# Performance work log

Measured on AMD Instinct MI355X. Metric: run time of the kernel, lower is better.

## Reference

```python
import jax, jax.numpy as jnp
import numpy as np

B, T, C = 2, 2048, 1024
H = 16
D = C // H  # head_dim = 64
EPS = 1e-06
MAX_SEQ = 2048


def make_rotary(dim, max_seq_len, base=10000):
    inv_freq = 1.0 / (base ** (jnp.arange(0, dim, 2, dtype=jnp.float32) / dim))
    pos = jnp.arange(max_seq_len, dtype=jnp.float32)
    sinusoid = jnp.einsum('i,j->ij', pos, inv_freq)  # (S, dim//2)
    return jnp.sin(sinusoid), jnp.cos(sinusoid)


def apply_rotary(x, sin, cos):
    # x: (B, T, H, D); sin/cos: (MAX_SEQ, D//2)
    t = x.shape[1]
    s = sin[:t][:, None, :]  # (T,1,D//2) broadcasts over B and H
    c = cos[:t][:, None, :]
    d = x.shape[-1]
    x1, x2 = x[..., :d // 2], x[..., d // 2:]
    return jnp.concatenate([x1 * c - x2 * s, x2 * c + x1 * s], axis=-1)


def yat_dense(x, kernel, bias, alpha, eps=EPS):
    # Yat layer: squared dot product over squared euclidean distance.
    dot = x @ kernel                                   # (..., out)
    x_sq = jnp.sum(x * x, axis=-1, keepdims=True)      # (..., 1)
    k_sq = jnp.sum(kernel * kernel, axis=0)            # (out,)
    dist = x_sq + k_sq - 2.0 * dot
    y = (dot * dot) / (dist + eps)
    out_f = kernel.shape[1]
    scale = (jnp.sqrt(jnp.float32(out_f)) / jnp.log(1.0 + jnp.float32(out_f))) ** alpha
    return y * scale + bias


def setup_inputs() -> dict:
    key = jax.random.key(0)
    ks = jax.random.split(key, 7)
    x = jax.random.normal(ks[0], (B, T, C), dtype=jnp.float32)
    mask = jnp.tril(jnp.ones((T, T), dtype=bool))[None].repeat(B, axis=0)  # (B,T,T) causal
    s = 1.0 / np.sqrt(C)
    w_attn = jax.random.normal(ks[1], (C, 3 * C), dtype=jnp.float32) * s
    b_attn = jnp.zeros((3 * C,), dtype=jnp.float32)
    a_attn = jnp.ones((1,), dtype=jnp.float32)
    w_proj = jax.random.normal(ks[2], (C, C), dtype=jnp.float32) * s
    b_proj = jnp.zeros((C,), dtype=jnp.float32)
    a_proj = jnp.ones((1,), dtype=jnp.float32)
    return {"x": x, "mask": mask, "w_attn": w_attn, "b_attn": b_attn,
            "a_attn": a_attn, "w_proj": w_proj, "b_proj": b_proj, "a_proj": a_proj}


def reference(x, mask, w_attn, b_attn, a_attn, w_proj, b_proj, a_proj):
    b, t, c = x.shape
    sin, cos = make_rotary(D, MAX_SEQ)
    qkv = yat_dense(x, w_attn, b_attn, a_attn)          # (B,T,3C)
    qkv = qkv.reshape(b, t, 3, H, D)
    q, k, v = jnp.moveaxis(qkv, 2, 0)                   # each (B,T,H,D)
    q = apply_rotary(q, sin, cos)
    k = apply_rotary(k, sin, cos)
    # heads-major layout for attention
    q = q.transpose(0, 2, 1, 3)                          # (B,H,T,D)
    k = k.transpose(0, 2, 1, 3)
    v = v.transpose(0, 2, 1, 3)
    scale = jnp.sqrt(jnp.float32(D))
    attn = jnp.einsum('bhqd,bhkd->bhqk', q, k) / scale   # (B,H,T,T)
    m = mask[:, None, :, :]                              # (B,1,T,T)
    attn = jnp.where(m, attn, jnp.finfo(jnp.float32).min)
    attn = jax.nn.softmax(attn, axis=-1)
    # dropout is identity in deterministic/eval mode
    out = jnp.einsum('bhqk,bhkd->bhqd', attn, v)         # (B,H,T,D)
    out = out.transpose(0, 2, 1, 3).reshape(b, t, c)     # (B,T,C)
    out = yat_dense(out, w_proj, b_proj, a_proj)
    return out
```

## Files before the change

kernel.cpp:

```cpp
#include <hip/hip_runtime.h>
#include <math.h>

#define TSEQ  2048
#define BATCH 2
#define NH    16
#define HD    64
#define CDIM  1024
#define N3C   3072
#define EPSY  1e-6f

typedef unsigned short u16;
typedef unsigned int u32;
typedef __attribute__((ext_vector_type(2))) unsigned int u32x2;
typedef __attribute__((ext_vector_type(8))) short bf16x8;
typedef __attribute__((ext_vector_type(4))) float f32x4;

#define MFMA16(a, b, c) __builtin_amdgcn_mfma_f32_16x16x32_bf16(a, b, c, 0, 0, 0)

__device__ __forceinline__ u16 f2bf(float f) {
    unsigned u = __float_as_uint(f);
    return (u16)((u + 0x7fffu + ((u >> 16) & 1u)) >> 16);
}
__device__ __forceinline__ u32 cvtpk_bf16(float lo, float hi) {
    u32 r;
    asm("v_cvt_pk_bf16_f32 %0, %1, %2" : "=v"(r) : "v"(lo), "v"(hi));
    return r;
}
__device__ __forceinline__ void gload16(const void* g, void* l) {
    __builtin_amdgcn_global_load_lds(
        (const __attribute__((address_space(1))) unsigned int*)g,
        (__attribute__((address_space(3))) unsigned int*)l, 16, 0, 0);
}

__global__ __launch_bounds__(256) void prep_kernel(
    const float* __restrict__ x, const float* __restrict__ wa,
    const float* __restrict__ wp, u16* __restrict__ Ahi,
    u16* __restrict__ Wthi, u16* __restrict__ Wphi,
    float* __restrict__ ksq, float* __restrict__ xsq,
    float* __restrict__ osq, float2* __restrict__ ropeSC) {
    __shared__ float smem[64 * 68];
    int bid = blockIdx.x, tid = threadIdx.x;

    if (bid < 4096) {
        int lane = tid & 63, wv = tid >> 6;
        size_t base = (size_t)bid * CDIM + tid * 4;
        float4 v = *(const float4*)(x + base);
        ushort4 hi;
        hi.x = f2bf(v.x); hi.y = f2bf(v.y); hi.z = f2bf(v.z); hi.w = f2bf(v.w);
        *(ushort4*)(Ahi + base) = hi;
        float s = v.x * v.x + v.y * v.y + v.z * v.z + v.w * v.w;
        #pragma unroll
        for (int off = 32; off; off >>= 1) s += __shfl_down(s, off, 64);
        if (lane == 0) smem[wv] = s;
        __syncthreads();
        if (tid == 0) xsq[bid] = smem[0] + smem[1] + smem[2] + smem[3];
    } else if (bid < 5120) {
        const float* W; u16* Whi; int K, N, bx, by;
        if (bid < 4864) {
            int t = bid - 4096; W = wa; Whi = Wthi; K = CDIM; N = N3C;
            bx = t % 48; by = t / 48;
        } else {
            int t = bid - 4864; W = wp; Whi = Wphi; K = CDIM; N = CDIM;
            bx = t % 16; by = t / 16;
        }
        int k0 = by * 64, n0 = bx * 64;
        int r = tid >> 4, c4 = (tid & 15) * 4;
        #pragma unroll
        for (int i = 0; i < 4; ++i) {
            int k = k0 + r + i * 16;
            float4 v = *(const float4*)(W + (size_t)k * N + n0 + c4);
            *(float4*)&smem[(r + i * 16) * 68 + c4] = v;
        }
        __syncthreads();
        int n = tid >> 4, k4 = (tid & 15) * 4;
        #pragma unroll
        for (int i = 0; i < 4; ++i) {
            int nn = n + i * 16;
            ushort4 hi;
            hi.x = f2bf(smem[(k4 + 0) * 68 + nn]);
            hi.y = f2bf(smem[(k4 + 1) * 68 + nn]);
            hi.z = f2bf(smem[(k4 + 2) * 68 + nn]);
            hi.w = f2bf(smem[(k4 + 3) * 68 + nn]);
            *(ushort4*)(Whi + (size_t)(n0 + nn) * K + k0 + k4) = hi;
        }
    } else if (bid < 5184) {
        int b2 = bid - 5120;
        int c = tid & 63, kq = tid >> 6;
        const float* W; int N, col, outoff;
        if (b2 < 48) { W = wa; N = N3C;  col = b2 * 64 + c;        outoff = 0;   }
        else         { W = wp; N = CDIM; col = (b2 - 48) * 64 + c; outoff = N3C; }
        float s = 0.f;
        int i0 = kq * 256;
        #pragma unroll 4
        for (int i = i0; i < i0 + 256; ++i) {
            float v = W[(size_t)i * N + col];
            s = fmaf(v, v, s);
        }
        smem[tid] = s;
        __syncthreads();
        if (kq == 0)
            ksq[outoff + col] = smem[c] + smem[64 + c] + smem[128 + c] + smem[192 + c];
    } else {
        int idx = (bid - 5184) * 256 + tid;
        if (idx < BATCH * TSEQ) osq[idx] = 0.f;
        int t = idx >> 5, j = idx & 31;
        float inv = exp2f(-(float)j * 0.4152410118609203f);
        float ang = (float)t * inv;
        ropeSC[idx] = make_float2(cosf(ang), sinf(ang));
    }
}

__global__ __launch_bounds__(256, 4) void gemm1_fused(
    const u16* __restrict__ Ah, const u16* __restrict__ Bh,
    const float* __restrict__ bias, const float* __restrict__ rowsq,
    const float* __restrict__ colsq, const float* __restrict__ alphap,
    const float2* __restrict__ ropeSC,
    u16* __restrict__ Qb, u16* __restrict__ Kb, u16* __restrict__ Vt) {
    constexpr int BK = 32;
    const int K = CDIM;
    __shared__ u16 Ash[2][128 * BK], Bsh[2][128 * BK];
    int tid = threadIdx.x;
    int lane = tid & 63, wv = tid >> 6;
    int quad = lane >> 4, l15 = lane & 15;
    int wr = wv >> 1, wc = wv & 1;
    int bm = blockIdx.y * 128, bn = blockIdx.x * 128;
    int rsub = lane >> 2;
    int lc8 = (lane & 3) * 8;
    int gc8 = (((lane & 3) - (rsub >> 1)) & 3) * 8;
    int pf8 = ((quad + (l15 >> 1)) & 3) * 8;

    f32x4 acc[4][4];
    #pragma unroll
    for (int i = 0; i < 4; ++i)
        #pragma unroll
        for (int j = 0; j < 4; ++j) acc[i][j] = (f32x4){0.f, 0.f, 0.f, 0.f};

    auto STAGE = [&](int buf, int kt) {
        #pragma unroll
        for (int i = 0; i < 2; ++i) {
            int r = i * 64 + wv * 16 + rsub;
            gload16(Ah + (size_t)(bm + r) * K + kt + gc8, &Ash[buf][r * BK + lc8]);
            gload16(Bh + (size_t)(bn + r) * K + kt + gc8, &Bsh[buf][r * BK + lc8]);
        }
    };

    STAGE(0, 0);
    __syncthreads();
    int cur = 0;

    for (int kt = 0; kt < K; kt += BK) {
        if (kt + BK < K) STAGE(cur ^ 1, kt + BK);
        bf16x8 fah[4], fbh[4];
        #pragma unroll
        for (int i = 0; i < 4; ++i)
            fah[i] = *(const bf16x8*)&Ash[cur][(wr * 64 + i * 16 + l15) * BK + pf8];
        #pragma unroll
        for (int j = 0; j < 4; ++j)
            fbh[j] = *(const bf16x8*)&Bsh[cur][(wc * 64 + j * 16 + l15) * BK + pf8];
        #pragma unroll
        for (int i = 0; i < 4; ++i)
            #pragma unroll
            for (int j = 0; j < 4; ++j)
                acc[i][j] = MFMA16(fah[i], fbh[j], acc[i][j]);
        __syncthreads();
        cur ^= 1;
    }

    float alpha = alphap[0];
    float scale = powf(sqrtf((float)N3C) / logf(1.0f + (float)N3C), alpha);
    int segc0 = bn + wc * 64;
    int seg = segc0 >> 10;
    int h = (segc0 >> 6) & 15;
    int bglob = bm >> 11;
    int bh = bglob * NH + h;

    if (seg < 2) {
        u16* dst = (seg == 0) ? Qb : Kb;
        float qs = (seg == 0) ? 0.18033688011112043f : 1.0f;
        #pragma unroll
        for (int i = 0; i < 4; ++i) {
            int tb = bm + wr * 64 + i * 16 + quad * 4;
            #pragma unroll
            for (int r = 0; r < 4; ++r) {
                int row = tb + r;
                int t = row & (TSEQ - 1);
                float rs = rowsq[row];
                float y[4];
                #pragma unroll
                for (int j = 0; j < 4; ++j) {
                    int col = segc0 + j * 16 + l15;
                    float dot = acc[i][j][r];
                    float dist = rs + colsq[col] - 2.0f * dot + EPSY;
                    y[j] = dot * dot / dist * scale + bias[col];
                }
                float2 sc0 = ropeSC[t * 32 + l15];
                float2 sc1 = ropeSC[t * 32 + 16 + l15];
                float c0 = sc0.x, s0 = sc0.y, c1 = sc1.x, s1 = sc1.y;
                size_t ob = ((size_t)bh * TSEQ + t) * HD;
                dst[ob + l15]      = f2bf((y[0] * c0 - y[2] * s0) * qs);
                dst[ob + 16 + l15] = f2bf((y[1] * c1 - y[3] * s1) * qs);
                dst[ob + 32 + l15] = f2bf((y[2] * c0 + y[0] * s0) * qs);
                dst[ob + 48 + l15] = f2bf((y[3] * c1 + y[1] * s1) * qs);
            }
        }
    } else {
        #pragma unroll
        for (int i = 0; i < 4; ++i) {
            int tb = bm + wr * 64 + i * 16 + quad * 4;
            int t0 = tb & (TSEQ - 1);
            #pragma unroll
            for (int j = 0; j < 4; ++j) {
                int col = segc0 + j * 16 + l15;
                int d = j * 16 + l15;
                float cs = colsq[col], bi = bias[col];
                ushort4 pk;
                u16* pp = (u16*)&pk;
                #pragma unroll
                for (int r = 0; r < 4; ++r) {
                    float dot = acc[i][j][r];
                    float dist = rowsq[tb + r] + cs - 2.0f * dot + EPSY;
                    pp[r] = f2bf(dot * dot / dist * scale + bi);
                }
                *(ushort4*)(Vt + ((size_t)bh * HD + d) * TSEQ + t0) = pk;
            }
        }
    }
}

__global__ __launch_bounds__(256, 4) void gemm_yat_mfma(
    const u16* __restrict__ Ah, const u16* __restrict__ Bh,
    const float* __restrict__ bias, const float* __restrict__ rowsq,
    const float* __restrict__ colsq, const float* __restrict__ alphap,
    float* __restrict__ outp, int M, int N, int K, float outf) {
    constexpr int BM = 128, BN = 64, BK = 32;
    __shared__ u16 Ash[2][BM * BK], Bsh[2][BN * BK];
    int tid = threadIdx.x;
    int lane = tid & 63, wv = tid >> 6;
    int quad = lane >> 4, l15 = lane & 15;
    int bm = blockIdx.y * BM, bn = blockIdx.x * BN;
    int rsub = lane >> 2;
    int lc8 = (lane & 3) * 8;
    int gc8 = (((lane & 3) - (rsub >> 1)) & 3) * 8;
    int pf8 = ((quad + (l15 >> 1)) & 3) * 8;

    f32x4 acc[2][4];
    #pragma unroll
    for (int i = 0; i < 2; ++i)
        #pragma unroll
        for (int j = 0; j < 4; ++j) acc[i][j] = (f32x4){0.f, 0.f, 0.f, 0.f};

    auto STAGE = [&](int buf, int kt) {
        #pragma unroll
        for (int i = 0; i < 2; ++i) {
            int r = i * 64 + wv * 16 + rsub;
            gload16(Ah + (size_t)(bm + r) * K + kt + gc8, &Ash[buf][r * BK + lc8]);
        }
        {
            int r = wv * 16 + rsub;
            gload16(Bh + (size_t)(bn + r) * K + kt + gc8, &Bsh[buf][r * BK + lc8]);
        }
    };

    STAGE(0, 0);
    __syncthreads();
    int cur = 0;

    for (int kt = 0; kt < K; kt += BK) {
        if (kt + BK < K) STAGE(cur ^ 1, kt + BK);
        bf16x8 fah[2], fbh[4];
        #pragma unroll
        for (int i = 0; i < 2; ++i)
            fah[i] = *(const bf16x8*)&Ash[cur][(wv * 32 + i * 16 + l15) * BK + pf8];
        #pragma unroll
        for (int j = 0; j < 4; ++j)
            fbh[j] = *(const bf16x8*)&Bsh[cur][(j * 16 + l15) * BK + pf8];
        #pragma unroll
        for (int i = 0; i < 2; ++i)
            #pragma unroll
            for (int j = 0; j < 4; ++j)
                acc[i][j] = MFMA16(fah[i], fbh[j], acc[i][j]);
        __syncthreads();
        cur ^= 1;
    }

    float alpha = alphap[0];
    float scale = powf(sqrtf(outf) / logf(1.0f + outf), alpha);
    #pragma unroll
    for (int j = 0; j < 4; ++j) {
        int col = bn + j * 16 + l15;
        float cs = colsq[col], bi = bias[col];
        #pragma unroll
        for (int i = 0; i < 2; ++i) {
            #pragma unroll
            for (int r = 0; r < 4; ++r) {
                int row = bm + wv * 32 + i * 16 + quad * 4 + r;
                float dot = acc[i][j][r];
                float dist = rowsq[row] + cs - 2.0f * dot + EPSY;
                outp[(size_t)row * N + col] = dot * dot / dist * scale + bi;
            }
        }
    }
}

__global__ __launch_bounds__(512) void attn_mfma(
    const u16* __restrict__ Qb, const u16* __restrict__ Kb,
    const u16* __restrict__ Vt, u16* __restrict__ Chi,
    float* __restrict__ osq) {
    __shared__ u16 Ksh[2][64 * 64];
    __shared__ u16 Vsh[2][64 * 64];
    int tid = threadIdx.x;
    int lane = tid & 63, wv = tid >> 6;
    int quad = lane >> 4, l15 = lane & 15;
    const bool oddq = (quad & 1) != 0;
    int bh = blockIdx.x;
    int b = bh >> 4, h = bh & 15;
    const u16* Qh = Qb + (size_t)bh * TSEQ * HD;
    const u16* Kh = Kb + (size_t)bh * TSEQ * HD;
    const u16* Vh = Vt + (size_t)bh * HD * TSEQ;
    const f32x4 zf = {0.f, 0.f, 0.f, 0.f};

    int qbb = 15 - blockIdx.y;
    int qw = qbb * 128 + wv * 16;
    int NT = 2 * qbb + 2;
    bf16x8 bq0 = *(const bf16x8*)(Qh + (size_t)(qw + l15) * HD + quad * 8);
    bf16x8 bq1 = *(const bf16x8*)(Qh + (size_t)(qw + l15) * HD + 32 + quad * 8);

    f32x4 o[4] = {zf, zf, zf, zf};
    float l = 0.f;

    auto STAGE = [&](int buf, int kt) {
        int k0s = kt * 64;
        int rowi = tid >> 3, ch = tid & 7;
        int gk = (ch + rowi) & 7;
        gload16(Kh + (size_t)(k0s + rowi) * HD + gk * 8, &Ksh[buf][tid * 8]);
        gload16(Vh + (size_t)rowi * TSEQ + k0s + gk * 8, &Vsh[buf][tid * 8]);
    };

    STAGE(0, 0);
    __syncthreads();
    int cur = 0;

    for (int kt = 0; kt < NT; ++kt) {
        int k0 = kt * 64;
        if (kt + 1 < NT) STAGE(cur ^ 1, kt + 1);
        if (k0 <= qw + 15) {
            const u16* Kc = Ksh[cur];
            const u16* Vc = Vsh[cur];

            f32x4 st[4];
            __builtin_amdgcn_s_setprio(1);
            #pragma unroll
            for (int mt = 0; mt < 4; ++mt) {
                int key = mt * 16 + l15;
                bf16x8 a0 = *(const bf16x8*)&Kc[key * 64 + ((quad - key) & 7) * 8];
                bf16x8 a1 = *(const bf16x8*)&Kc[key * 64 + ((4 + quad - key) & 7) * 8];
                st[mt] = MFMA16(a0, bq0, zf);
                st[mt] = MFMA16(a1, bq1, st[mt]);
            }
            __builtin_amdgcn_s_setprio(0);
            if (k0 + 63 > qw) {
                int q = qw + l15;
                #pragma unroll
                for (int mt = 0; mt < 4; ++mt)
                    #pragma unroll
                    for (int r = 0; r < 4; ++r)
                        if (k0 + mt * 16 + quad * 4 + r > q) st[mt][r] = -1e30f;
            }
            u32 pp[4][2];
            #pragma unroll
            for (int mt = 0; mt < 4; ++mt) {
                float p0 = __builtin_amdgcn_exp2f(st[mt][0]);
                float p1 = __builtin_amdgcn_exp2f(st[mt][1]);
                float p2 = __builtin_amdgcn_exp2f(st[mt][2]);
                float p3 = __builtin_amdgcn_exp2f(st[mt][3]);
                l += (p0 + p1) + (p2 + p3);
                pp[mt][0] = cvtpk_bf16(p0, p1);
                pp[mt][1] = cvtpk_bf16(p2, p3);
            }
            #pragma unroll
            for (int s = 0; s < 2; ++s) {
                u32x2 r0 = __builtin_amdgcn_permlane32_swap(
                    pp[2 * s][0], pp[2 * s + 1][0], false, false);
                u32 sA0 = (u32)__builtin_amdgcn_ds_swizzle((int)r0.x, 0x401F);
                u32 sB0 = (u32)__builtin_amdgcn_ds_swizzle((int)r0.y, 0x401F);
                u32x2 r1 = __builtin_amdgcn_permlane32_swap(
                    pp[2 * s][1], pp[2 * s + 1][1], false, false);
                u32 sA1 = (u32)__builtin_amdgcn_ds_swizzle((int)r1.x, 0x401F);
                u32 sB1 = (u32)__builtin_amdgcn_ds_swizzle((int)r1.y, 0x401F);
                u32 bw0 = oddq ? sB0 : r0.x;
                u32 bw1 = oddq ? sB1 : r1.x;
                u32 bw2 = oddq ? r0.y : sA0;
                u32 bw3 = oddq ? r1.y : sA1;
                bf16x8 bfr;
                *(u32*)&((short*)&bfr)[0] = bw0;
                *(u32*)&((short*)&bfr)[2] = bw1;
                *(u32*)&((short*)&bfr)[4] = bw2;
                *(u32*)&((short*)&bfr)[6] = bw3;
                __builtin_amdgcn_s_setprio(1);
                #pragma unroll
                for (int dt = 0; dt < 4; ++dt) {
                    int d = dt * 16 + l15;
                    bf16x8 av = *(const bf16x8*)&Vc[d * 64 + ((s * 4 + quad - d) & 7) * 8];
                    o[dt] = MFMA16(av, bfr, o[dt]);
                }
                __builtin_amdgcn_s_setprio(0);
            }
        }
        __syncthreads();
        cur ^= 1;
    }

    l += __shfl_xor(l, 16, 64);
    l += __shfl_xor(l, 32, 64);
    float inv = 1.0f / l;
    int row = (b << 11) + qw + l15;
    float ss = 0.f;
    #pragma unroll
    for (int dt = 0; dt < 4; ++dt) {
        float v0 = o[dt][0] * inv, v1 = o[dt][1] * inv;
        float v2 = o[dt][2] * inv, v3 = o[dt][3] * inv;
        ss += v0 * v0 + v1 * v1 + v2 * v2 + v3 * v3;
        uint2 pk2;
        pk2.x = cvtpk_bf16(v0, v1);
        pk2.y = cvtpk_bf16(v2, v3);
        *(uint2*)(Chi + (size_t)row * CDIM + h * HD + dt * 16 + quad * 4) = pk2;
    }
    ss += __shfl_xor(ss, 16, 64);
    ss += __shfl_xor(ss, 32, 64);
    if (quad == 0) atomicAdd(osq + row, ss);
}

extern "C" void kernel_launch(void* const* d_in, const int* in_sizes, int n_in,
                              void* d_out, int out_size, void* d_ws, size_t ws_size,
                              hipStream_t stream) {
    const float* x      = (const float*)d_in[0];
    const float* w_attn = (const float*)d_in[2];
    const float* b_attn = (const float*)d_in[3];
    const float* a_attn = (const float*)d_in[4];
    const float* w_proj = (const float*)d_in[5];
    const float* b_proj = (const float*)d_in[6];
    const float* a_proj = (const float*)d_in[7];
    float* outp = (float*)d_out;

    char* ws = (char*)d_ws;
    float* ksq = (float*)(ws);
    float* xsq = (float*)(ws + 16384);
    float* osq = (float*)(ws + 32768);
    char* pA  = ws + 65536;
    u16* Ahi = (u16*)pA;
    u16* Chi = (u16*)pA;
    char* pWt = pA + 16777216;
    u16* Wthi = (u16*)pWt;
    char* pWp = pWt + 6291456;
    u16* Wphi = (u16*)pWp;
    char* pQ = pWp + 2097152;
    u16* Qb = (u16*)pQ;
    u16* Kb = (u16*)(pQ + 8388608);
    u16* Vt = (u16*)(pQ + 16777216);
    float2* ropeSC = (float2*)(pQ + 25165824);

    prep_kernel<<<5440, 256, 0, stream>>>(
        x, w_attn, w_proj, Ahi, Wthi, Wphi, ksq, xsq, osq, ropeSC);
    gemm1_fused<<<dim3(N3C / 128, (BATCH * TSEQ) / 128), 256, 0, stream>>>(
        Ahi, Wthi, b_attn, xsq, ksq, a_attn, ropeSC, Qb, Kb, Vt);
    attn_mfma<<<dim3(BATCH * NH, 16), 512, 0, stream>>>(Qb, Kb, Vt, Chi, osq);
    gemm_yat_mfma<<<dim3(CDIM / 64, (BATCH * TSEQ) / 128), 256, 0, stream>>>(
        Chi, Wphi, b_proj, osq, ksq + N3C, a_proj, outp,
        BATCH * TSEQ, CDIM, CDIM, (float)CDIM);
}
```

Before: 225.6 us.

## Retile QKV GEMM to 128x64 blocks with two waves and swizzle block order

The fused QKV GEMM now uses 128x64 output tiles computed by 128-thread blocks (two waves, each owning 64 rows). This doubles the grid to 1536 blocks so more of the machine's CUs get work. Both GEMMs also remap the linear block index with a stride-8 swizzle, which changes which blocks run together and is meant to improve L2 reuse of the A and B tiles. In exchange each block carries a smaller B tile, so operand reuse per block drops and total global traffic rises.

```diff
diff --git a/kernel.cpp b/kernel.cpp
--- a/kernel.cpp
+++ b/kernel.cpp
@@ -110,7 +110,7 @@
     }
 }
 
-__global__ __launch_bounds__(256, 4) void gemm1_fused(
+__global__ __launch_bounds__(128, 3) void gemm1_fused(
     const u16* __restrict__ Ah, const u16* __restrict__ Bh,
     const float* __restrict__ bias, const float* __restrict__ rowsq,
     const float* __restrict__ colsq, const float* __restrict__ alphap,
@@ -118,15 +118,20 @@
     u16* __restrict__ Qb, u16* __restrict__ Kb, u16* __restrict__ Vt) {
     constexpr int BK = 32;
     const int K = CDIM;
-    __shared__ u16 Ash[2][128 * BK], Bsh[2][128 * BK];
+    __shared__ u16 Ash[2][128 * BK], Bsh[2][64 * BK];
     int tid = threadIdx.x;
     int lane = tid & 63, wv = tid >> 6;
     int quad = lane >> 4, l15 = lane & 15;
-    int wr = wv >> 1, wc = wv & 1;
-    int bm = blockIdx.y * 128, bn = blockIdx.x * 128;
-    int rsub = lane >> 2;
-    int lc8 = (lane & 3) * 8;
-    int gc8 = (((lane & 3) - (rsub >> 1)) & 3) * 8;
+
+    int lin = blockIdx.x + blockIdx.y * 48;
+    int swz = (lin & 7) * 192 + (lin >> 3);
+    int bn = (swz % 48) * 64;
+    int bm = (swz / 48) * 128;
+
+    int rs = tid >> 2;
+    int cc = tid & 3;
+    int lc8 = cc * 8;
+    int gc8 = ((cc - ((rs & 15) >> 1)) & 3) * 8;
     int pf8 = ((quad + (l15 >> 1)) & 3) * 8;
 
     f32x4 acc[4][4];
@@ -137,9 +142,13 @@
 
     auto STAGE = [&](int buf, int kt) {
         #pragma unroll
-        for (int i = 0; i < 2; ++i) {
-            int r = i * 64 + wv * 16 + rsub;
+        for (int p = 0; p < 4; ++p) {
+            int r = p * 32 + rs;
             gload16(Ah + (size_t)(bm + r) * K + kt + gc8, &Ash[buf][r * BK + lc8]);
+        }
+        #pragma unroll
+        for (int p = 0; p < 2; ++p) {
+            int r = p * 32 + rs;
             gload16(Bh + (size_t)(bn + r) * K + kt + gc8, &Bsh[buf][r * BK + lc8]);
         }
     };
@@ -153,10 +162,10 @@
         bf16x8 fah[4], fbh[4];
         #pragma unroll
         for (int i = 0; i < 4; ++i)
-            fah[i] = *(const bf16x8*)&Ash[cur][(wr * 64 + i * 16 + l15) * BK + pf8];
+            fah[i] = *(const bf16x8*)&Ash[cur][(wv * 64 + i * 16 + l15) * BK + pf8];
         #pragma unroll
         for (int j = 0; j < 4; ++j)
-            fbh[j] = *(const bf16x8*)&Bsh[cur][(wc * 64 + j * 16 + l15) * BK + pf8];
+            fbh[j] = *(const bf16x8*)&Bsh[cur][(j * 16 + l15) * BK + pf8];
         #pragma unroll
         for (int i = 0; i < 4; ++i)
             #pragma unroll
@@ -168,7 +177,7 @@
 
     float alpha = alphap[0];
     float scale = powf(sqrtf((float)N3C) / logf(1.0f + (float)N3C), alpha);
-    int segc0 = bn + wc * 64;
+    int segc0 = bn;
     int seg = segc0 >> 10;
     int h = (segc0 >> 6) & 15;
     int bglob = bm >> 11;
@@ -179,18 +188,18 @@
         float qs = (seg == 0) ? 0.18033688011112043f : 1.0f;
         #pragma unroll
         for (int i = 0; i < 4; ++i) {
-            int tb = bm + wr * 64 + i * 16 + quad * 4;
+            int tb = bm + wv * 64 + i * 16 + quad * 4;
             #pragma unroll
             for (int r = 0; r < 4; ++r) {
                 int row = tb + r;
                 int t = row & (TSEQ - 1);
-                float rs = rowsq[row];
+                float rs2 = rowsq[row];
                 float y[4];
                 #pragma unroll
                 for (int j = 0; j < 4; ++j) {
                     int col = segc0 + j * 16 + l15;
                     float dot = acc[i][j][r];
-                    float dist = rs + colsq[col] - 2.0f * dot + EPSY;
+                    float dist = rs2 + colsq[col] - 2.0f * dot + EPSY;
                     y[j] = dot * dot / dist * scale + bias[col];
                 }
                 float2 sc0 = ropeSC[t * 32 + l15];
@@ -206,7 +215,7 @@
     } else {
         #pragma unroll
         for (int i = 0; i < 4; ++i) {
-            int tb = bm + wr * 64 + i * 16 + quad * 4;
+            int tb = bm + wv * 64 + i * 16 + quad * 4;
             int t0 = tb & (TSEQ - 1);
             #pragma unroll
             for (int j = 0; j < 4; ++j) {
@@ -237,7 +246,10 @@
     int tid = threadIdx.x;
     int lane = tid & 63, wv = tid >> 6;
     int quad = lane >> 4, l15 = lane & 15;
-    int bm = blockIdx.y * BM, bn = blockIdx.x * BN;
+    int lin = blockIdx.x + blockIdx.y * 16;
+    int swz = (lin & 7) * 64 + (lin >> 3);
+    int bn = (swz % 16) * BN;
+    int bm = (swz / 16) * BM;
     int rsub = lane >> 2;
     int lc8 = (lane & 3) * 8;
     int gc8 = (((lane & 3) - (rsub >> 1)) & 3) * 8;
@@ -461,7 +473,7 @@
 
     prep_kernel<<<5440, 256, 0, stream>>>(
         x, w_attn, w_proj, Ahi, Wthi, Wphi, ksq, xsq, osq, ropeSC);
-    gemm1_fused<<<dim3(N3C / 128, (BATCH * TSEQ) / 128), 256, 0, stream>>>(
+    gemm1_fused<<<dim3(N3C / 64, (BATCH * TSEQ) / 128), 128, 0, stream>>>(
         Ahi, Wthi, b_attn, xsq, ksq, a_attn, ropeSC, Qb, Kb, Vt);
     attn_mfma<<<dim3(BATCH * NH, 16), 512, 0, stream>>>(Qb, Kb, Vt, Chi, osq);
     gemm_yat_mfma<<<dim3(CDIM / 64, (BATCH * TSEQ) / 128), 256, 0, stream>>>(
```

Measured after the change: 233.3 us. 1.03x slower.
